# Performance work log

Measured on AMD Instinct MI355X. Metric: run time of the kernel, lower is better.

## Reference

```python
import jax, jax.numpy as jnp
import numpy as np

N = 100000   # nodes
E = 640000   # directed edges
H = 128      # hidden_channels
C = 7        # dataset_num_classes
G = 64       # graphs in the batch
F_IN = 1     # dataset_num_node_features


def setup_inputs() -> dict:
    key = jax.random.key(0)
    ks = jax.random.split(key, 12)
    x = jax.random.normal(ks[0], (N, F_IN), jnp.float32)
    edge_index = jax.random.randint(ks[1], (2, E), 0, N, dtype=jnp.int32)
    batch = jnp.sort(jax.random.randint(ks[2], (N,), 0, G, dtype=jnp.int32))

    def glorot(k, fan_in, fan_out):
        s = jnp.sqrt(6.0 / (fan_in + fan_out)).astype(jnp.float32)
        return jax.random.uniform(k, (fan_in, fan_out), jnp.float32, -s, s)

    return {
        "x": x, "edge_index": edge_index, "batch": batch,
        "W1": glorot(ks[3], F_IN, H), "b1": jnp.zeros((H,), jnp.float32),
        "W2": glorot(ks[4], H, H),    "b2": jnp.zeros((H,), jnp.float32),
        "W3": glorot(ks[5], H, H),    "b3": jnp.zeros((H,), jnp.float32),
        "Wl": glorot(ks[6], H, C),    "bl": jnp.zeros((C,), jnp.float32),
    }


def reference(x, edge_index, batch, W1, b1, W2, b2, W3, b3, Wl, bl):
    n = x.shape[0]
    loop = jnp.arange(n, dtype=edge_index.dtype)
    row = jnp.concatenate([edge_index[0], loop])  # source (message origin)
    col = jnp.concatenate([edge_index[1], loop])  # target (aggregation dst)
    # symmetric normalization D^-1/2 (A+I) D^-1/2 (PyG GCNConv default)
    deg = jax.ops.segment_sum(jnp.ones(row.shape[0], x.dtype), col, num_segments=n)
    dinv = jax.lax.rsqrt(jnp.maximum(deg, 1.0))  # deg >= 1 due to self-loops
    norm = dinv[row] * dinv[col]                 # [E+N]

    def gcn_conv(h, W, b):
        h = h @ W                                # transform first (PyG order)
        msg = h[row] * norm[:, None]             # gather + scale, [E+N, H]
        return jax.ops.segment_sum(msg, col, num_segments=n) + b

    h = jax.nn.relu(gcn_conv(x, W1, b1))
    h = jax.nn.relu(gcn_conv(h, W2, b2))
    h = gcn_conv(h, W3, b3)

    # global mean pool over graph ids; dropout is identity in eval mode
    counts = jax.ops.segment_sum(jnp.ones(n, h.dtype), batch, num_segments=G)
    pooled = jax.ops.segment_sum(h, batch, num_segments=G) / jnp.maximum(counts, 1.0)[:, None]
    return pooled @ Wl + bl
```

## Files before the change

kernel.cpp:

```cpp
#include <hip/hip_runtime.h>

#define HDIM 128
#define NGRAPH 64
#define NCLASS 7
#define MAXB 2048

typedef __attribute__((ext_vector_type(8))) __bf16 bf16x8;
typedef __attribute__((ext_vector_type(4))) float f32x4;

__device__ __forceinline__ unsigned short bf16_rne(float f) {
  unsigned u = __float_as_uint(f);
  u += 0x7FFF + ((u >> 16) & 1);
  return (unsigned short)(u >> 16);
}

__device__ __forceinline__ void gload16(const void* g, void* l) {
  __builtin_amdgcn_global_load_lds((const __attribute__((address_space(1))) void*)g,
                                   (__attribute__((address_space(3))) void*)l, 16, 0, 0);
}


__global__ void k_countw(const int* __restrict__ col, const int* __restrict__ row, int E,
                         int* __restrict__ histI, int* __restrict__ histO,
                         const float* __restrict__ W,
                         unsigned short* __restrict__ wthi, unsigned short* __restrict__ wtlo,
                         int cB, int NB) {
  int b = blockIdx.x;
  if (b < cB) {
    __shared__ int binsI[MAXB], binsO[MAXB];
    int t = threadIdx.x;
    for (int i = t; i < NB; i += 256) { binsI[i] = 0; binsO[i] = 0; }
    __syncthreads();
    int base = b << 11;
#pragma unroll
    for (int j = 0; j < 8; j++) {
      int e = base + (j << 8) + t;
      if (e < E) {
        atomicAdd(&binsI[col[e] >> 6], 1);
        atomicAdd(&binsO[row[e] >> 6], 1);
      }
    }
    __syncthreads();
    for (int i = t; i < NB; i += 256) {
      histI[(size_t)b * NB + i] = binsI[i];
      histO[(size_t)b * NB + i] = binsO[i];
    }
  } else {
    int idx = (b - cB) * 256 + threadIdx.x;
    int c = idx >> 7, k = idx & 127;
    float v = W[k * 128 + c];
    unsigned short h = bf16_rne(v);
    wthi[idx] = h;
    wtlo[idx] = bf16_rne(v - __uint_as_float((unsigned)h << 16));
  }
}

__global__ void k_hA(int* __restrict__ histI, int* __restrict__ histO,
                     int* __restrict__ segI, int* __restrict__ segO,
                     int NB, int cB) {
  int bkt = blockIdx.x * 256 + threadIdx.x;
  if (bkt >= NB) return;
  int* hist = blockIdx.z ? histO : histI;
  int* segs = blockIdx.z ? segO : segI;
  int r0 = blockIdx.y << 3;
  int v[8];
#pragma unroll
  for (int j = 0; j < 8; j++) {
    int ri = r0 + j;
    v[j] = (ri < cB) ? hist[(size_t)ri * NB + bkt] : 0;
  }
  int s = 0;
#pragma unroll
  for (int j = 0; j < 8; j++) { int tv = v[j]; v[j] = s; s += tv; }
#pragma unroll
  for (int j = 0; j < 8; j++) {
    int ri = r0 + j;
    if (ri < cB) hist[(size_t)ri * NB + bkt] = v[j];
  }
  segs[(size_t)blockIdx.y * NB + bkt] = s;
}

__global__ void k_hB(int* __restrict__ segI, int* __restrict__ segO,
                     int* __restrict__ btotI, int* __restrict__ btotO,
                     int NB, int NSEG) {
  int bkt = blockIdx.x * 256 + threadIdx.x;
  if (bkt >= NB) return;
  int* segs = blockIdx.y ? segO : segI;
  int* btot = blockIdx.y ? btotO : btotI;
  int run = 0;
  for (int c0 = 0; c0 < NSEG; c0 += 8) {
    int v[8];
#pragma unroll
    for (int j = 0; j < 8; j++) {
      int si = c0 + j;
      v[j] = (si < NSEG) ? segs[(size_t)si * NB + bkt] : 0;
    }
#pragma unroll
    for (int j = 0; j < 8; j++) { int tv = v[j]; v[j] = run; run += tv; }
#pragma unroll
    for (int j = 0; j < 8; j++) {
      int si = c0 + j;
      if (si < NSEG) segs[(size_t)si * NB + bkt] = v[j];
    }
  }
  btot[bkt] = run;
}

__global__ void k_hscanB(const int* __restrict__ btotI, int* __restrict__ boffI,
                         const int* __restrict__ btotO, int* __restrict__ boffO,
                         int NB, int E) {
  __shared__ int sh[1024];
  int t = threadIdx.x;
  for (int s = 0; s < 2; s++) {
    const int* src = s ? btotO : btotI;
    int* boff = s ? boffO : boffI;
    int i0 = 2 * t, i1 = 2 * t + 1;
    int a0 = (i0 < NB) ? src[i0] : 0;
    int a1 = (i1 < NB) ? src[i1] : 0;
    sh[t] = a0 + a1;
    __syncthreads();
    for (int o = 1; o < 1024; o <<= 1) {
      int v = (t >= o) ? sh[t - o] : 0;
      __syncthreads();
      sh[t] += v;
      __syncthreads();
    }
    int ex = (t == 0) ? 0 : sh[t - 1];
    if (i0 < NB) boff[i0] = ex;
    if (i1 < NB) boff[i1] = ex + a0;
    if (t == 0) boff[NB] = E;
    __syncthreads();
  }
}

__global__ void __launch_bounds__(256) k_fill(const int* __restrict__ row,
                                              const int* __restrict__ col, int E,
                                              const int* __restrict__ histI,
                                              const int* __restrict__ histO,
                                              const int* __restrict__ segI,
                                              const int* __restrict__ segO,
                                              const int* __restrict__ boffI,
                                              const int* __restrict__ boffO,
                                              int* __restrict__ inBL,
                                              int* __restrict__ outBL, int NB) {
  __shared__ int baseI[MAXB], baseO[MAXB], binsI[MAXB], binsO[MAXB];
  int t = threadIdx.x, b = blockIdx.x;
  int sg = b >> 3;
  for (int i = t; i < NB; i += 256) {
    baseI[i] = boffI[i] + segI[(size_t)sg * NB + i] + histI[(size_t)b * NB + i];
    baseO[i] = boffO[i] + segO[(size_t)sg * NB + i] + histO[(size_t)b * NB + i];
    binsI[i] = 0;
    binsO[i] = 0;
  }
  __syncthreads();
  int base = b << 11;
#pragma unroll
  for (int j = 0; j < 8; j++) {
    int e = base + (j << 8) + t;
    if (e < E) {
      int r = row[e], c = col[e];
      int rkI = atomicAdd(&binsI[c >> 6], 1);
      int rkO = atomicAdd(&binsO[r >> 6], 1);
      inBL[baseI[c >> 6] + rkI] = (r << 6) | (c & 63);
      outBL[baseO[r >> 6] + rkO] = (c << 6) | (r & 63);
    }
  }
}

__global__ void __launch_bounds__(256) k_rank2x(const int* __restrict__ inBL,
                                                const int* __restrict__ boffI,
                                                const int* __restrict__ batch,
                                                const float* __restrict__ x,
                                                int2* __restrict__ od,
                                                float2* __restrict__ dx,
                                                int* __restrict__ gwi, int n) {
  __shared__ int cnt[64], cnt2[64], loc[64], sc[64];
  int bi = blockIdx.x, t = threadIdx.x;
  if (t < 64) { cnt[t] = 0; cnt2[t] = 0; }
  __syncthreads();
  int e0 = boffI[bi], e1 = boffI[bi + 1];
  for (int e = e0 + t; e < e1; e += 256) atomicAdd(&cnt[inBL[e] & 63], 1);
  __syncthreads();
  if (t < 64) sc[t] = cnt[t];
  __syncthreads();
  for (int o = 1; o < 64; o <<= 1) {
    int v = (t < 64 && t >= o) ? sc[t - o] : 0;
    __syncthreads();
    if (t < 64) sc[t] += v;
    __syncthreads();
  }
  if (t < 64) {
    int excl = (t == 0) ? 0 : sc[t - 1];
    loc[t] = e0 + excl;
    int node = (bi << 6) + t;
    if (node < n) {
      int g = batch[node];
      float dinv = rsqrtf((float)(cnt[t] + 1));
      od[node] = make_int2((e0 + excl) | (g << 24), __float_as_int(dinv));
      dx[node] = make_float2(dinv, x[node]);
    }
  }
  __syncthreads();
  for (int e = e0 + t; e < e1; e += 256) {
    int v = inBL[e];
    int dl = v & 63;
    int k = atomicAdd(&cnt2[dl], 1);
    gwi[loc[dl] + k] = v >> 6;
  }
}

__global__ void k_s(const int2* __restrict__ od, const float2* __restrict__ dx,
                    const int* __restrict__ gwi, float2* __restrict__ sd, int n, int E) {
  int i = blockIdx.x * 256 + threadIdx.x;
  if (i >= n) return;
  int2 o2 = od[i];
  float dinv = __int_as_float(o2.y);
  int e0 = o2.x & 0xFFFFFF;
  int e1 = (i + 1 < n) ? (od[i + 1].x & 0xFFFFFF) : E;
  float s0 = 0.f, s1 = 0.f;
  int e = e0;
  for (; e + 2 <= e1; e += 2) {
    float2 a = dx[gwi[e]];
    float2 b = dx[gwi[e + 1]];
    s0 = fmaf(a.x, a.y, s0);
    s1 = fmaf(b.x, b.y, s1);
  }
  if (e < e1) { float2 a = dx[gwi[e]]; s0 = fmaf(a.x, a.y, s0); }
  float xv = dx[i].y;
  sd[i] = make_float2(fmaf(dinv * dinv, xv, dinv * (s0 + s1)), dinv);
}


__global__ void __launch_bounds__(256) k_l2in(const float2* __restrict__ sd,
                                              const int2* __restrict__ od,
                                              const int* __restrict__ gwi,
                                              const float* __restrict__ W1,
                                              const float* __restrict__ b1,
                                              ushort2* __restrict__ zhi,
                                              ushort2* __restrict__ zlo, int n, int E) {
  int node = blockIdx.x * 4 + (threadIdx.x >> 6);
  if (node >= n) return;
  int l = threadIdx.x & 63;
  float2 w1 = ((const float2*)W1)[l];
  float2 bv = ((const float2*)b1)[l];
  int2 on = od[node];
  float dstd = __int_as_float(on.y);
  float nself = dstd * dstd;
  float sv = sd[node].x;
  float2 acc;
  acc.x = nself * fmaxf(fmaf(sv, w1.x, bv.x), 0.f);
  acc.y = nself * fmaxf(fmaf(sv, w1.y, bv.y), 0.f);
  int e0 = on.x & 0xFFFFFF;
  int e1 = (node + 1 < n) ? (od[node + 1].x & 0xFFFFFF) : E;

  for (int eb = e0; eb < e1; eb += 64) {
    int m = e1 - eb; if (m > 64) m = 64;
    int ee = eb + l; if (ee >= e1) ee = e1 - 1;
    float2 q = sd[gwi[ee]];
    float u = q.y * dstd;
    int k = 0;
    for (; k + 4 <= m; k += 4) {
      float q0 = __shfl(q.x, k),     u0 = __shfl(u, k);
      float q1 = __shfl(q.x, k + 1), u1 = __shfl(u, k + 1);
      float q2 = __shfl(q.x, k + 2), u2 = __shfl(u, k + 2);
      float q3 = __shfl(q.x, k + 3), u3 = __shfl(u, k + 3);
      acc.x = fmaf(u0, fmaxf(fmaf(q0, w1.x, bv.x), 0.f), acc.x);
      acc.y = fmaf(u0, fmaxf(fmaf(q0, w1.y, bv.y), 0.f), acc.y);
      acc.x = fmaf(u1, fmaxf(fmaf(q1, w1.x, bv.x), 0.f), acc.x);
      acc.y = fmaf(u1, fmaxf(fmaf(q1, w1.y, bv.y), 0.f), acc.y);
      acc.x = fmaf(u2, fmaxf(fmaf(q2, w1.x, bv.x), 0.f), acc.x);
      acc.y = fmaf(u2, fmaxf(fmaf(q2, w1.y, bv.y), 0.f), acc.y);
      acc.x = fmaf(u3, fmaxf(fmaf(q3, w1.x, bv.x), 0.f), acc.x);
      acc.y = fmaf(u3, fmaxf(fmaf(q3, w1.y, bv.y), 0.f), acc.y);
    }
    for (; k < m; k++) {
      float qk = __shfl(q.x, k), uk = __shfl(u, k);
      acc.x = fmaf(uk, fmaxf(fmaf(qk, w1.x, bv.x), 0.f), acc.x);
      acc.y = fmaf(uk, fmaxf(fmaf(qk, w1.y, bv.y), 0.f), acc.y);
    }
  }

  ushort2 h, lo;
  h.x = bf16_rne(acc.x);
  lo.x = bf16_rne(acc.x - __uint_as_float((unsigned)h.x << 16));
  h.y = bf16_rne(acc.y);
  lo.y = bf16_rne(acc.y - __uint_as_float((unsigned)h.y << 16));
  zhi[(size_t)node * 64 + l] = h;
  zlo[(size_t)node * 64 + l] = lo;
}


union SmemU {
  uint4 stage[2048];
  struct { float Hf[64 * 128]; float Pl[64 * 64]; } pg;
};

__global__ void __launch_bounds__(256)
k_gemm_pg(const unsigned short* __restrict__ zhi, const unsigned short* __restrict__ zlo,
          const unsigned short* __restrict__ whi, const unsigned short* __restrict__ wlo,
          const float* __restrict__ bias, const int* __restrict__ outBL,
          const int* __restrict__ boffO, const int2* __restrict__ od,
          float* __restrict__ partials, int n) {
  __shared__ SmemU u;
  __shared__ float dinvL[128];
  const int t = threadIdx.x;
  const int l = t & 63, wv = t >> 6;
  const int wr = wv >> 1, wc = wv & 1;
  const int lr = l & 15, lk = l >> 4;
  const int rowBase = blockIdx.x << 7;
  const bool full = (rowBase + 128 <= n);

  f32x4 acc[4][4];
#pragma unroll
  for (int mt = 0; mt < 4; mt++)
#pragma unroll
    for (int nt = 0; nt < 4; nt++) acc[mt][nt] = (f32x4){0.f, 0.f, 0.f, 0.f};

  for (int ch = 0; ch < 4; ch++) {
    __syncthreads();
    if (full) {
#pragma unroll
      for (int i = 0; i < 2; i++) {
        int s = t + (i << 8);
        int sl = s & 63, rt = s >> 6;
        int row = rowBase + (rt << 4) + (sl & 15);
        int kk = (ch << 5) + ((sl >> 4) << 3);
        gload16(&zhi[(size_t)row * 128 + kk], &u.stage[s]);
        gload16(&zlo[(size_t)row * 128 + kk], &u.stage[512 + s]);
      }
    } else {
#pragma unroll
      for (int i = 0; i < 2; i++) {
        int s = t + (i << 8);
        int sl = s & 63, rt = s >> 6;
        int row = rowBase + (rt << 4) + (sl & 15);
        int kk = (ch << 5) + ((sl >> 4) << 3);
        uint4 vh = make_uint4(0u, 0u, 0u, 0u), vl = vh;
        if (row < n) {
          vh = *(const uint4*)&zhi[(size_t)row * 128 + kk];
          vl = *(const uint4*)&zlo[(size_t)row * 128 + kk];
        }
        u.stage[s] = vh;
        u.stage[512 + s] = vl;
      }
    }
#pragma unroll
    for (int i = 0; i < 2; i++) {
      int s = t + (i << 8);
      int sl = s & 63, ct = s >> 6;
      int col = (ct << 4) + (sl & 15);
      int kk = (ch << 5) + ((sl >> 4) << 3);
      gload16(&whi[col * 128 + kk], &u.stage[1024 + s]);
      gload16(&wlo[col * 128 + kk], &u.stage[1536 + s]);
    }
    __syncthreads();

    bf16x8 ah[4], al[4], bh[4], bl[4];
#pragma unroll
    for (int mt = 0; mt < 4; mt++) {
      int slot = ((wr << 2) + mt) * 64 + l;
      ah[mt] = *(const bf16x8*)&u.stage[slot];
      al[mt] = *(const bf16x8*)&u.stage[512 + slot];
    }
#pragma unroll
    for (int nt = 0; nt < 4; nt++) {
      int slot = ((wc << 2) + nt) * 64 + l;
      bh[nt] = *(const bf16x8*)&u.stage[1024 + slot];
      bl[nt] = *(const bf16x8*)&u.stage[1536 + slot];
    }
#pragma unroll
    for (int mt = 0; mt < 4; mt++)
#pragma unroll
      for (int nt = 0; nt < 4; nt++) {
        acc[mt][nt] = __builtin_amdgcn_mfma_f32_16x16x32_bf16(ah[mt], bh[nt], acc[mt][nt], 0, 0, 0);
        acc[mt][nt] = __builtin_amdgcn_mfma_f32_16x16x32_bf16(ah[mt], bl[nt], acc[mt][nt], 0, 0, 0);
        acc[mt][nt] = __builtin_amdgcn_mfma_f32_16x16x32_bf16(al[mt], bh[nt], acc[mt][nt], 0, 0, 0);
      }
  }

  float bv[4];
#pragma unroll
  for (int nt = 0; nt < 4; nt++) bv[nt] = bias[(wc << 6) + (nt << 4) + lr];
#pragma unroll
  for (int mt = 0; mt < 4; mt++)
#pragma unroll
    for (int nt = 0; nt < 4; nt++)
#pragma unroll
      for (int j = 0; j < 4; j++)
        acc[mt][nt][j] = fmaxf(acc[mt][nt][j] + bv[nt], 0.f);

  if (t < 128) {
    int node = rowBase + t;
    dinvL[t] = (node < n) ? __int_as_float(od[node].y) : 0.f;
  }

  const int jl = t & 31;
  const int gq = (t >> 5) << 1;
  float4 acc2[8];
#pragma unroll
  for (int i = 0; i < 8; i++) acc2[i] = make_float4(0.f, 0.f, 0.f, 0.f);

  for (int sub = 0; sub < 2; sub++) {
    const int base = rowBase + (sub << 6);
    __syncthreads();
    for (int i4 = t; i4 < 1024; i4 += 256)
      ((float4*)u.pg.Pl)[i4] = make_float4(0.f, 0.f, 0.f, 0.f);
    if (wr == sub) {
#pragma unroll
      for (int mt = 0; mt < 4; mt++)
#pragma unroll
        for (int j = 0; j < 4; j++) {
          int li = (mt << 4) + (lk << 2) + j;
          bool ok = (base + li) < n;
#pragma unroll
          for (int nt = 0; nt < 4; nt++)
            u.pg.Hf[li * 128 + (wc << 6) + (nt << 4) + lr] = ok ? acc[mt][nt][j] : 0.f;
        }
    }
    __syncthreads();
    if (t < 64) {
      int node = base + t;
      if (node < n) {
        float dv = dinvL[(sub << 6) + t];
        atomicAdd(&u.pg.Pl[(t << 6) + (int)(((unsigned)od[node].x) >> 24)], dv * dv);
      }
    }
    int e0 = 0, e1 = 0;
    if (base < n) {
      int bi = base >> 6;
      e0 = boffO[bi];
      e1 = boffO[bi + 1];
    }
    const float* dL = &dinvL[sub << 6];
    for (int e = e0 + t; e < e1; e += 256) {
      int p = outBL[e];
      int2 oc = od[p >> 6];
      float w2 = dL[p & 63] * __int_as_float(oc.y);
      atomicAdd(&u.pg.Pl[((p & 63) << 6) + (int)(((unsigned)oc.x) >> 24)], w2);
    }
    __syncthreads();

#define FMA4(A, PV) \
  A.x = fmaf(PV, hv.x, A.x); A.y = fmaf(PV, hv.y, A.y); \
  A.z = fmaf(PV, hv.z, A.z); A.w = fmaf(PV, hv.w, A.w);
#pragma unroll 4
    for (int i = 0; i < 64; i++) {
      float4 hv = *(const float4*)&u.pg.Hf[i * 128 + (jl << 2)];
      float4 pa = ((const float4*)u.pg.Pl)[i * 16 + gq];
      float4 pb = ((const float4*)u.pg.Pl)[i * 16 + gq + 1];
      FMA4(acc2[0], pa.x) FMA4(acc2[1], pa.y) FMA4(acc2[2], pa.z) FMA4(acc2[3], pa.w)
      FMA4(acc2[4], pb.x) FMA4(acc2[5], pb.y) FMA4(acc2[6], pb.z) FMA4(acc2[7], pb.w)
    }
#undef FMA4
  }

  float* dst = &partials[(size_t)blockIdx.x * (NGRAPH * HDIM)];
  int gb = (t >> 5) << 3;
#pragma unroll
  for (int gi = 0; gi < 8; gi++)
    *(float4*)&dst[(gb + gi) * HDIM + (jl << 2)] = acc2[gi];
}

__global__ void k_reduce(const float* __restrict__ partials, float* __restrict__ pooled,
                         int nparts) {
  int cell = blockIdx.x * 256 + threadIdx.x;
  int stride = gridDim.y;
  int p = blockIdx.y;
  float a0 = 0.f, a1 = 0.f, a2 = 0.f, a3 = 0.f;
  for (; p + 3 * stride < nparts; p += 4 * stride) {
    a0 += partials[(size_t)p * 8192 + cell];
    a1 += partials[(size_t)(p + stride) * 8192 + cell];
    a2 += partials[(size_t)(p + 2 * stride) * 8192 + cell];
    a3 += partials[(size_t)(p + 3 * stride) * 8192 + cell];
  }
  for (; p < nparts; p += stride) a0 += partials[(size_t)p * 8192 + cell];
  unsafeAtomicAdd(&pooled[cell], (a0 + a1) + (a2 + a3));
}

__global__ void k_mid(const float* __restrict__ pooled, const int* __restrict__ batch, int n,
                      const float* __restrict__ W3, const float* __restrict__ b3,
                      const float* __restrict__ Wl, const float* __restrict__ bl,
                      float* __restrict__ out) {
  __shared__ float sh[HDIM];
  __shared__ float invSh;
  int g = blockIdx.x, j = threadIdx.x;
  if (j == 0) {
    int lo = 0, hi = n;
    while (lo < hi) { int m = (lo + hi) >> 1; if (batch[m] < g) lo = m + 1; else hi = m; }
    int a = lo;
    lo = 0; hi = n;
    while (lo < hi) { int m = (lo + hi) >> 1; if (batch[m] < g + 1) lo = m + 1; else hi = m; }
    invSh = 1.f / fmaxf((float)(lo - a), 1.f);
  }
  __syncthreads();
  float inv = invSh;
  float acc = 0.f;
  for (int k = 0; k < HDIM; k++) acc = fmaf(pooled[g * HDIM + k], W3[k * HDIM + j], acc);
  sh[j] = acc * inv + b3[j];
  __syncthreads();
  if (j < NCLASS) {
    float o = bl[j];
    for (int k = 0; k < HDIM; k++) o = fmaf(sh[k], Wl[k * NCLASS + j], o);
    out[g * NCLASS + j] = o;
  }
}


extern "C" void kernel_launch(void* const* d_in, const int* in_sizes, int n_in,
                              void* d_out, int out_size, void* d_ws, size_t ws_size,
                              hipStream_t stream) {
  const float* x   = (const float*)d_in[0];
  const int*   ei  = (const int*)d_in[1];
  const int*   bat = (const int*)d_in[2];
  const float* W1  = (const float*)d_in[3];
  const float* b1  = (const float*)d_in[4];
  const float* W2  = (const float*)d_in[5];
  const float* b2  = (const float*)d_in[6];
  const float* W3  = (const float*)d_in[7];
  const float* b3  = (const float*)d_in[8];
  const float* Wl  = (const float*)d_in[9];
  const float* bl  = (const float*)d_in[10];
  float* out = (float*)d_out;

  const int n = in_sizes[0];
  const int E = in_sizes[1] / 2;
  const int* rowv = ei;
  const int* colv = ei + E;
  const int NB = (n + 63) >> 6;
  const int cB = (E + 2047) / 2048;
  const int NSEG = (cB + 7) >> 3;
  const int nPB = (n + 127) >> 7;

  char* w = (char*)d_ws;
  size_t o = 0;
  auto alloc = [&](size_t bytes) {
    size_t r = (o + 255) & ~(size_t)255;
    o = r + bytes;
    return r;
  };

  size_t o_pool  = alloc((size_t)NGRAPH * HDIM * 4);
  size_t zero_end = o;
  size_t o_histI = alloc((size_t)cB * NB * 4);
  size_t o_histO = alloc((size_t)cB * NB * 4);
  size_t o_segI  = alloc((size_t)NSEG * NB * 4);
  size_t o_segO  = alloc((size_t)NSEG * NB * 4);
  size_t o_btotI = alloc((size_t)MAXB * 4);
  size_t o_btotO = alloc((size_t)MAXB * 4);
  size_t o_boffI = alloc((size_t)(MAXB + 1) * 4);
  size_t o_boffO = alloc((size_t)(MAXB + 1) * 4);
  size_t o_od    = alloc((size_t)n * 8);
  size_t o_dx    = alloc((size_t)n * 8);
  size_t o_sd    = alloc((size_t)n * 8);
  size_t o_wt    = alloc((size_t)HDIM * HDIM * 4);
  size_t o_gw    = alloc((size_t)E * 4);
  size_t o_inBL  = alloc((size_t)E * 4);
  size_t o_outBL = alloc((size_t)E * 4);
  size_t o_part  = alloc((size_t)nPB * NGRAPH * HDIM * 4);
  size_t o_bufB  = alloc((size_t)n * HDIM * 4);
  (void)n_in; (void)out_size; (void)ws_size;

  float*  pooled   = (float*)(w + o_pool);
  int*    histI    = (int*)(w + o_histI);
  int*    histO    = (int*)(w + o_histO);
  int*    segI     = (int*)(w + o_segI);
  int*    segO     = (int*)(w + o_segO);
  int*    btotI    = (int*)(w + o_btotI);
  int*    btotO    = (int*)(w + o_btotO);
  int*    boffI    = (int*)(w + o_boffI);
  int*    boffO    = (int*)(w + o_boffO);
  int2*   od       = (int2*)(w + o_od);
  float2* dx       = (float2*)(w + o_dx);
  float2* sd       = (float2*)(w + o_sd);
  unsigned short* wthi = (unsigned short*)(w + o_wt);
  unsigned short* wtlo = wthi + HDIM * HDIM;
  int*    gwi      = (int*)(w + o_gw);
  int*    inBL     = (int*)(w + o_inBL);
  int*    outBL    = (int*)(w + o_outBL);
  float*  partials = (float*)(w + o_part);
  unsigned short* zhi = (unsigned short*)(w + o_bufB);
  unsigned short* zlo = zhi + (size_t)n * HDIM;

  hipMemsetAsync(w + o_pool, 0, zero_end - o_pool, stream);

  const int gB = (NB + 255) / 256;
  k_countw<<<cB + 64, 256, 0, stream>>>(colv, rowv, E, histI, histO, W2,
                                        wthi, wtlo, cB, NB);
  k_hA<<<dim3(gB, NSEG, 2), 256, 0, stream>>>(histI, histO, segI, segO, NB, cB);
  k_hB<<<dim3(gB, 2), 256, 0, stream>>>(segI, segO, btotI, btotO, NB, NSEG);
  k_hscanB<<<1, 1024, 0, stream>>>(btotI, boffI, btotO, boffO, NB, E);
  k_fill<<<cB, 256, 0, stream>>>(rowv, colv, E, histI, histO, segI, segO,
                                 boffI, boffO, inBL, outBL, NB);
  k_rank2x<<<NB, 256, 0, stream>>>(inBL, boffI, bat, x, od, dx, gwi, n);
  k_s<<<(n + 255) / 256, 256, 0, stream>>>(od, dx, gwi, sd, n, E);

  k_l2in<<<(n + 3) / 4, 256, 0, stream>>>(sd, od, gwi, W1, b1,
                                          (ushort2*)zhi, (ushort2*)zlo, n, E);

  k_gemm_pg<<<nPB, 256, 0, stream>>>(zhi, zlo, wthi, wtlo, b2, outBL, boffO, od,
                                     partials, n);
  k_reduce<<<dim3(32, 8), 256, 0, stream>>>(partials, pooled, nPB);

  k_mid<<<NGRAPH, HDIM, 0, stream>>>(pooled, bat, n, W3, b3, Wl, bl, out);
}
```

Before: 243.2 us.

## Halve pooling LDS buffer by staging hidden columns in two passes

The pooling stage in the fused GEMM+pool kernel now stages the 64x128 activation tile into shared memory as two 64x64 halves, one per column-half wave group, instead of all at once. Each thread owns 4 graphs by 4 columns in each half rather than 8 graphs by 4 columns. This shrinks the LDS union from 48 KB to 32 KB (the staging area now sets the size), which could allow more resident blocks per CU. The cost is extra __syncthreads barriers and two passes over the pooling matrix.

New measurement: 248.6 us. 2.2% more time.

```diff
diff --git a/kernel.cpp b/kernel.cpp
--- a/kernel.cpp
+++ b/kernel.cpp
@@ -292,7 +292,7 @@
 
 union SmemU {
   uint4 stage[2048];
-  struct { float Hf[64 * 128]; float Pl[64 * 64]; } pg;
+  struct { float Hf[64 * 64]; float Pl[64 * 64]; } pg;
 };
 
 __global__ void __launch_bounds__(256)
@@ -394,8 +394,8 @@
     dinvL[t] = (node < n) ? __int_as_float(od[node].y) : 0.f;
   }
 
-  const int jl = t & 31;
-  const int gq = (t >> 5) << 1;
+  const int jq = t & 15;
+  const int gg = (t >> 4) << 2;
   float4 acc2[8];
 #pragma unroll
   for (int i = 0; i < 8; i++) acc2[i] = make_float4(0.f, 0.f, 0.f, 0.f);
@@ -405,7 +405,8 @@
     __syncthreads();
     for (int i4 = t; i4 < 1024; i4 += 256)
       ((float4*)u.pg.Pl)[i4] = make_float4(0.f, 0.f, 0.f, 0.f);
-    if (wr == sub) {
+    __syncthreads();
+    if (wr == sub && wc == 0) {
 #pragma unroll
       for (int mt = 0; mt < 4; mt++)
 #pragma unroll
@@ -414,10 +415,9 @@
           bool ok = (base + li) < n;
 #pragma unroll
           for (int nt = 0; nt < 4; nt++)
-            u.pg.Hf[li * 128 + (wc << 6) + (nt << 4) + lr] = ok ? acc[mt][nt][j] : 0.f;
+            u.pg.Hf[li * 64 + (nt << 4) + lr] = ok ? acc[mt][nt][j] : 0.f;
         }
     }
-    __syncthreads();
     if (t < 64) {
       int node = base + t;
       if (node < n) {
@@ -445,20 +445,39 @@
   A.z = fmaf(PV, hv.z, A.z); A.w = fmaf(PV, hv.w, A.w);
 #pragma unroll 4
     for (int i = 0; i < 64; i++) {
-      float4 hv = *(const float4*)&u.pg.Hf[i * 128 + (jl << 2)];
-      float4 pa = ((const float4*)u.pg.Pl)[i * 16 + gq];
-      float4 pb = ((const float4*)u.pg.Pl)[i * 16 + gq + 1];
+      float4 hv = *(const float4*)&u.pg.Hf[i * 64 + (jq << 2)];
+      float4 pa = *(const float4*)&u.pg.Pl[i * 64 + gg];
       FMA4(acc2[0], pa.x) FMA4(acc2[1], pa.y) FMA4(acc2[2], pa.z) FMA4(acc2[3], pa.w)
-      FMA4(acc2[4], pb.x) FMA4(acc2[5], pb.y) FMA4(acc2[6], pb.z) FMA4(acc2[7], pb.w)
+    }
+    __syncthreads();
+    if (wr == sub && wc == 1) {
+#pragma unroll
+      for (int mt = 0; mt < 4; mt++)
+#pragma unroll
+        for (int j = 0; j < 4; j++) {
+          int li = (mt << 4) + (lk << 2) + j;
+          bool ok = (base + li) < n;
+#pragma unroll
+          for (int nt = 0; nt < 4; nt++)
+            u.pg.Hf[li * 64 + (nt << 4) + lr] = ok ? acc[mt][nt][j] : 0.f;
+        }
+    }
+    __syncthreads();
+#pragma unroll 4
+    for (int i = 0; i < 64; i++) {
+      float4 hv = *(const float4*)&u.pg.Hf[i * 64 + (jq << 2)];
+      float4 pa = *(const float4*)&u.pg.Pl[i * 64 + gg];
+      FMA4(acc2[4], pa.x) FMA4(acc2[5], pa.y) FMA4(acc2[6], pa.z) FMA4(acc2[7], pa.w)
     }
 #undef FMA4
   }
 
   float* dst = &partials[(size_t)blockIdx.x * (NGRAPH * HDIM)];
-  int gb = (t >> 5) << 3;
-#pragma unroll
-  for (int gi = 0; gi < 8; gi++)
-    *(float4*)&dst[(gb + gi) * HDIM + (jl << 2)] = acc2[gi];
+#pragma unroll
+  for (int jh = 0; jh < 2; jh++)
+#pragma unroll
+    for (int gi = 0; gi < 4; gi++)
+      *(float4*)&dst[(gg + gi) * HDIM + (jh << 6) + (jq << 2)] = acc2[(jh << 2) + gi];
 }
 
 __global__ void k_reduce(const float* __restrict__ partials, float* __restrict__ pooled,
```

## Double k_gemm_pg block size to 512 threads, halving per-thread tile work

Applied to the files above, without the earlier changes.

Launches the fused GEMM+pooling kernel with 512 threads instead of 256, giving each wave a 32x64 output tile (2x4 MFMA tiles) instead of 64x64, and halving the per-thread accumulators in the pooling stage. Each thread now issues one staged load per matrix instead of two, and the edge loop strides by 512. The aim is lower register pressure and more waves per CU to hide latency. The cost is more threads per block sharing the same LDS stage and barriers, with less work per wave.

Result: faster. 235.0 us, median of 2 (-3.3%).

```diff
diff --git a/kernel.cpp b/kernel.cpp
--- a/kernel.cpp
+++ b/kernel.cpp
@@ -295,7 +295,7 @@
   struct { float Hf[64 * 128]; float Pl[64 * 64]; } pg;
 };
 
-__global__ void __launch_bounds__(256)
+__global__ void __launch_bounds__(512, 5)
 k_gemm_pg(const unsigned short* __restrict__ zhi, const unsigned short* __restrict__ zlo,
           const unsigned short* __restrict__ whi, const unsigned short* __restrict__ wlo,
           const float* __restrict__ bias, const int* __restrict__ outBL,
@@ -310,79 +310,62 @@
   const int rowBase = blockIdx.x << 7;
   const bool full = (rowBase + 128 <= n);
 
-  f32x4 acc[4][4];
-#pragma unroll
-  for (int mt = 0; mt < 4; mt++)
+  f32x4 acc[2][4];
+#pragma unroll
+  for (int mt = 0; mt < 2; mt++)
 #pragma unroll
     for (int nt = 0; nt < 4; nt++) acc[mt][nt] = (f32x4){0.f, 0.f, 0.f, 0.f};
 
   for (int ch = 0; ch < 4; ch++) {
     __syncthreads();
-    if (full) {
-#pragma unroll
-      for (int i = 0; i < 2; i++) {
-        int s = t + (i << 8);
-        int sl = s & 63, rt = s >> 6;
-        int row = rowBase + (rt << 4) + (sl & 15);
-        int kk = (ch << 5) + ((sl >> 4) << 3);
-        gload16(&zhi[(size_t)row * 128 + kk], &u.stage[s]);
-        gload16(&zlo[(size_t)row * 128 + kk], &u.stage[512 + s]);
-      }
-    } else {
-#pragma unroll
-      for (int i = 0; i < 2; i++) {
-        int s = t + (i << 8);
-        int sl = s & 63, rt = s >> 6;
-        int row = rowBase + (rt << 4) + (sl & 15);
-        int kk = (ch << 5) + ((sl >> 4) << 3);
+    {
+      int sl = t & 63, rt = t >> 6;
+      int row = rowBase + (rt << 4) + (sl & 15);
+      int kk = (ch << 5) + ((sl >> 4) << 3);
+      if (full) {
+        gload16(&zhi[(size_t)row * 128 + kk], &u.stage[t]);
+        gload16(&zlo[(size_t)row * 128 + kk], &u.stage[512 + t]);
+      } else {
         uint4 vh = make_uint4(0u, 0u, 0u, 0u), vl = vh;
         if (row < n) {
           vh = *(const uint4*)&zhi[(size_t)row * 128 + kk];
           vl = *(const uint4*)&zlo[(size_t)row * 128 + kk];
         }
-        u.stage[s] = vh;
-        u.stage[512 + s] = vl;
+        u.stage[t] = vh;
+        u.stage[512 + t] = vl;
       }
-    }
-#pragma unroll
-    for (int i = 0; i < 2; i++) {
-      int s = t + (i << 8);
-      int sl = s & 63, ct = s >> 6;
-      int col = (ct << 4) + (sl & 15);
-      int kk = (ch << 5) + ((sl >> 4) << 3);
-      gload16(&whi[col * 128 + kk], &u.stage[1024 + s]);
-      gload16(&wlo[col * 128 + kk], &u.stage[1536 + s]);
-    }
-    __syncthreads();
-
-    bf16x8 ah[4], al[4], bh[4], bl[4];
-#pragma unroll
-    for (int mt = 0; mt < 4; mt++) {
-      int slot = ((wr << 2) + mt) * 64 + l;
+      int col = (rt << 4) + (sl & 15);
+      gload16(&whi[col * 128 + kk], &u.stage[1024 + t]);
+      gload16(&wlo[col * 128 + kk], &u.stage[1536 + t]);
+    }
+    __syncthreads();
+
+    bf16x8 ah[2], al[2];
+#pragma unroll
+    for (int mt = 0; mt < 2; mt++) {
+      int slot = ((wr << 1) + mt) * 64 + l;
       ah[mt] = *(const bf16x8*)&u.stage[slot];
       al[mt] = *(const bf16x8*)&u.stage[512 + slot];
     }
 #pragma unroll
     for (int nt = 0; nt < 4; nt++) {
       int slot = ((wc << 2) + nt) * 64 + l;
-      bh[nt] = *(const bf16x8*)&u.stage[1024 + slot];
-      bl[nt] = *(const bf16x8*)&u.stage[1536 + slot];
-    }
-#pragma unroll
-    for (int mt = 0; mt < 4; mt++)
-#pragma unroll
-      for (int nt = 0; nt < 4; nt++) {
-        acc[mt][nt] = __builtin_amdgcn_mfma_f32_16x16x32_bf16(ah[mt], bh[nt], acc[mt][nt], 0, 0, 0);
-        acc[mt][nt] = __builtin_amdgcn_mfma_f32_16x16x32_bf16(ah[mt], bl[nt], acc[mt][nt], 0, 0, 0);
-        acc[mt][nt] = __builtin_amdgcn_mfma_f32_16x16x32_bf16(al[mt], bh[nt], acc[mt][nt], 0, 0, 0);
+      bf16x8 bh = *(const bf16x8*)&u.stage[1024 + slot];
+      bf16x8 bl = *(const bf16x8*)&u.stage[1536 + slot];
+#pragma unroll
+      for (int mt = 0; mt < 2; mt++) {
+        acc[mt][nt] = __builtin_amdgcn_mfma_f32_16x16x32_bf16(ah[mt], bh, acc[mt][nt], 0, 0, 0);
+        acc[mt][nt] = __builtin_amdgcn_mfma_f32_16x16x32_bf16(ah[mt], bl, acc[mt][nt], 0, 0, 0);
+        acc[mt][nt] = __builtin_amdgcn_mfma_f32_16x16x32_bf16(al[mt], bh, acc[mt][nt], 0, 0, 0);
       }
+    }
   }
 
   float bv[4];
 #pragma unroll
   for (int nt = 0; nt < 4; nt++) bv[nt] = bias[(wc << 6) + (nt << 4) + lr];
 #pragma unroll
-  for (int mt = 0; mt < 4; mt++)
+  for (int mt = 0; mt < 2; mt++)
 #pragma unroll
     for (int nt = 0; nt < 4; nt++)
 #pragma unroll
@@ -395,22 +378,22 @@
   }
 
   const int jl = t & 31;
-  const int gq = (t >> 5) << 1;
-  float4 acc2[8];
-#pragma unroll
-  for (int i = 0; i < 8; i++) acc2[i] = make_float4(0.f, 0.f, 0.f, 0.f);
+  const int gh = t >> 5;
+  float4 acc2[4];
+#pragma unroll
+  for (int i = 0; i < 4; i++) acc2[i] = make_float4(0.f, 0.f, 0.f, 0.f);
 
   for (int sub = 0; sub < 2; sub++) {
     const int base = rowBase + (sub << 6);
     __syncthreads();
-    for (int i4 = t; i4 < 1024; i4 += 256)
+    for (int i4 = t; i4 < 1024; i4 += 512)
       ((float4*)u.pg.Pl)[i4] = make_float4(0.f, 0.f, 0.f, 0.f);
-    if (wr == sub) {
-#pragma unroll
-      for (int mt = 0; mt < 4; mt++)
+    if ((wr >> 1) == sub) {
+#pragma unroll
+      for (int mt = 0; mt < 2; mt++)
 #pragma unroll
         for (int j = 0; j < 4; j++) {
-          int li = (mt << 4) + (lk << 2) + j;
+          int li = ((wr & 1) << 5) + (mt << 4) + (lk << 2) + j;
           bool ok = (base + li) < n;
 #pragma unroll
           for (int nt = 0; nt < 4; nt++)
@@ -432,7 +415,7 @@
       e1 = boffO[bi + 1];
     }
     const float* dL = &dinvL[sub << 6];
-    for (int e = e0 + t; e < e1; e += 256) {
+    for (int e = e0 + t; e < e1; e += 512) {
       int p = outBL[e];
       int2 oc = od[p >> 6];
       float w2 = dL[p & 63] * __int_as_float(oc.y);
@@ -446,19 +429,16 @@
 #pragma unroll 4
     for (int i = 0; i < 64; i++) {
       float4 hv = *(const float4*)&u.pg.Hf[i * 128 + (jl << 2)];
-      float4 pa = ((const float4*)u.pg.Pl)[i * 16 + gq];
-      float4 pb = ((const float4*)u.pg.Pl)[i * 16 + gq + 1];
+      float4 pa = ((const float4*)u.pg.Pl)[i * 16 + gh];
       FMA4(acc2[0], pa.x) FMA4(acc2[1], pa.y) FMA4(acc2[2], pa.z) FMA4(acc2[3], pa.w)
-      FMA4(acc2[4], pb.x) FMA4(acc2[5], pb.y) FMA4(acc2[6], pb.z) FMA4(acc2[7], pb.w)
     }
 #undef FMA4
   }
 
   float* dst = &partials[(size_t)blockIdx.x * (NGRAPH * HDIM)];
-  int gb = (t >> 5) << 3;
-#pragma unroll
-  for (int gi = 0; gi < 8; gi++)
-    *(float4*)&dst[(gb + gi) * HDIM + (jl << 2)] = acc2[gi];
+#pragma unroll
+  for (int gi = 0; gi < 4; gi++)
+    *(float4*)&dst[((gh << 2) + gi) * HDIM + (jl << 2)] = acc2[gi];
 }
 
 __global__ void k_reduce(const float* __restrict__ partials, float* __restrict__ pooled,
@@ -597,7 +577,7 @@
   k_l2in<<<(n + 3) / 4, 256, 0, stream>>>(sd, od, gwi, W1, b1,
                                           (ushort2*)zhi, (ushort2*)zlo, n, E);
 
-  k_gemm_pg<<<nPB, 256, 0, stream>>>(zhi, zlo, wthi, wtlo, b2, outBL, boffO, od,
+  k_gemm_pg<<<nPB, 512, 0, stream>>>(zhi, zlo, wthi, wtlo, b2, outBL, boffO, od,
                                      partials, n);
   k_reduce<<<dim3(32, 8), 256, 0, stream>>>(partials, pooled, nPB);
 
```
